# Performance work log

Hardware: AMD Instinct MI355X
Metric: run time of the kernel (lower is better)

Reference implementation:

```python
import jax, jax.numpy as jnp
import numpy as np

IN_DIM = 256
OUT_DIM = 256

def setup_inputs() -> dict:
    key = jax.random.key(0)
    k1, k2, k3, k4 = jax.random.split(key, 4)
    B, N, K, D = 4, 10000, 16, IN_DIM
    x = jax.random.normal(k1, (B, N, D), dtype=jnp.float32)
    neigh = jax.random.randint(k2, (N, K), 0, N, dtype=jnp.int64)
    # nn.Linear(2*in_dim, out_dim): W [out, 2*in], b [out]
    bound = 1.0 / np.sqrt(2 * D)
    W = jax.random.uniform(k3, (OUT_DIM, 2 * D), minval=-bound, maxval=bound, dtype=jnp.float32)
    b = jax.random.uniform(k4, (OUT_DIM,), minval=-bound, maxval=bound, dtype=jnp.float32)
    return {"x": x, "neigh": neigh, "W": W, "b": b}

def reference(x, neigh, W, b):
    # x: [B,N,D], neigh: [N,K] with -1 = padding
    mask = (neigh >= 0)                                # [N,K]
    idx = jnp.clip(neigh, 0, None)                     # [N,K]
    # batch_gather_nodes: x_nei[b,n,k,:] = x[b, idx[n,k], :]
    x_nei = x[:, idx, :]                               # [B,N,K,D]
    x_nei = x_nei * mask[None, :, :, None].astype(x.dtype)
    denom = jnp.clip(mask.sum(axis=1), 1, None).astype(x.dtype)  # [N]
    agg = x_nei.sum(axis=2) / denom[None, :, None]     # [B,N,D]
    h = jnp.concatenate([x, agg], axis=-1)             # [B,N,2D]
    return jax.nn.relu(jnp.einsum('bnd,od->bno', h, W) + b)
```

## Files before the change

kernel.cpp:

```cpp
#include <hip/hip_runtime.h>
#include <hip/hip_bf16.h>
#include <stdint.h>

#define B_   4
#define N_   10000
#define K_   16
#define D_   256
#define OUT_ 256
#define KDIM 512
#define M_   (B_ * N_)
#define CW   32
#define NCH  8

typedef __attribute__((ext_vector_type(8))) short          short8;
typedef __attribute__((ext_vector_type(8))) unsigned short ushort8;
typedef __attribute__((ext_vector_type(4))) float          f32x4;
typedef __attribute__((ext_vector_type(4))) unsigned short ushort4_t;

__device__ inline unsigned short f2bf(float f) {
    __hip_bfloat16 h = __float2bfloat16(f);
    return *reinterpret_cast<unsigned short*>(&h);
}
__device__ inline float bf2f(unsigned short u) {
    unsigned int v = ((unsigned int)u) << 16;
    return __builtin_bit_cast(float, v);
}

__global__ __launch_bounds__(256) void prep(const float* __restrict__ x,
                                            const float* __restrict__ W,
                                            unsigned short* __restrict__ h,
                                            unsigned short* __restrict__ xc,
                                            unsigned short* __restrict__ Wb) {
    const int t = threadIdx.x;
    if (blockIdx.x < 5000) {
        const int n  = blockIdx.x * 2 + (t >> 7);
        const int b  = (t >> 5) & 3;
        const int c0 = (t & 31) * 8;
        const float4* xr = (const float4*)(x + ((size_t)b * N_ + n) * D_ + c0);
        float4 v0 = xr[0];
        float4 v1 = xr[1];
        ushort8 s;
        s[0] = f2bf(v0.x); s[1] = f2bf(v0.y); s[2] = f2bf(v0.z); s[3] = f2bf(v0.w);
        s[4] = f2bf(v1.x); s[5] = f2bf(v1.y); s[6] = f2bf(v1.z); s[7] = f2bf(v1.w);
        *(ushort8*)(h + ((size_t)b * N_ + n) * KDIM + c0) = s;
        const int ch  = c0 >> 5;
        const int col = c0 & 31;
        *(ushort8*)(xc + (((size_t)ch * N_ + n) * B_ + b) * CW + col) = s;
    } else {
        int g = (blockIdx.x - 5000) * 256 + t;
        float4 v = ((const float4*)W)[g];
        ushort4_t s;
        s.x = f2bf(v.x); s.y = f2bf(v.y); s.z = f2bf(v.z); s.w = f2bf(v.w);
        ((ushort4_t*)Wb)[g] = s;
    }
}

__global__ __launch_bounds__(256) void gather_agg(const unsigned short* __restrict__ xc,
                                                  const int*            __restrict__ neigh,
                                                  unsigned short*       __restrict__ h) {
    const int c   = blockIdx.x & 7;
    const int g   = blockIdx.x >> 3;
    const int n0  = g * 8;
    const int tid = threadIdx.x;

    __shared__ int   idx_s[8 * K_];
    __shared__ float inv_s[8];

    if (tid < 8 * K_) idx_s[tid] = neigh[n0 * K_ + tid];
    __syncthreads();
    if (tid < 8) {
        int cnt = 0;
#pragma unroll
        for (int k = 0; k < K_; ++k) cnt += idx_s[tid * K_ + k] >= 0 ? 1 : 0;
        inv_s[tid] = 1.0f / (float)(cnt > 1 ? cnt : 1);
    }
    __syncthreads();

    const int q  = tid & 7;
    const int tl = tid >> 3;
    const int ns = tl >> 2;
    const int b  = tl & 3;

    const unsigned short* xcc = xc + (size_t)c * N_ * B_ * CW;

    int jj[K_];
#pragma unroll
    for (int k = 0; k < K_; ++k) jj[k] = idx_s[ns * K_ + k];

    ushort4_t vv[K_];
#pragma unroll
    for (int k = 0; k < K_; ++k) {
        const int jc = jj[k] >= 0 ? jj[k] : 0;
        vv[k] = *(const ushort4_t*)(xcc + ((size_t)jc * B_ + b) * CW + q * 4);
    }

    float a0 = 0.f, a1 = 0.f, a2 = 0.f, a3 = 0.f;
#pragma unroll
    for (int k = 0; k < K_; ++k) {
        const float m = jj[k] >= 0 ? 1.f : 0.f;
        a0 += bf2f(vv[k].x) * m;
        a1 += bf2f(vv[k].y) * m;
        a2 += bf2f(vv[k].z) * m;
        a3 += bf2f(vv[k].w) * m;
    }
    const float inv = inv_s[ns];

    ushort4_t s;
    s.x = f2bf(a0 * inv); s.y = f2bf(a1 * inv);
    s.z = f2bf(a2 * inv); s.w = f2bf(a3 * inv);
    *(ushort4_t*)(h + ((size_t)b * N_ + n0 + ns) * KDIM + D_ + c * CW + q * 4) = s;
}

__global__ __launch_bounds__(256) void gemm_bt2(const unsigned short* __restrict__ A,
                                                const unsigned short* __restrict__ Bm,
                                                const float* __restrict__ bias,
                                                float* __restrict__ out) {
    __shared__ unsigned short As[64 * 32];
    __shared__ unsigned short Bs[256 * 32];

    const int tid    = threadIdx.x;
    const int w      = tid >> 6;
    const int lane   = tid & 63;
    const int tile_m = blockIdx.x * 64;
    const int q      = lane >> 4;
    const int r16    = lane & 15;

    f32x4 acc[4][4] = {};

    const int crow = lane >> 2;
    const int kofs = (lane & 3) * 8;

    for (int kk = 0; kk < KDIM; kk += 32) {
#pragma unroll
        for (int t = 0; t < 5; ++t) {
            const int c = w * 5 + t;
            if (c < 4) {
                const int row = c * 16 + crow;
                const unsigned short* ga = A + (size_t)(tile_m + row) * KDIM + kk + kofs;
                __builtin_amdgcn_global_load_lds(
                    (const __attribute__((address_space(1))) void*)ga,
                    (__attribute__((address_space(3))) void*)(As + c * 512),
                    16, 0, 0);
            } else {
                const int row = (c - 4) * 16 + crow;
                const unsigned short* gb = Bm + (size_t)row * KDIM + kk + kofs;
                __builtin_amdgcn_global_load_lds(
                    (const __attribute__((address_space(1))) void*)gb,
                    (__attribute__((address_space(3))) void*)(Bs + (c - 4) * 512),
                    16, 0, 0);
            }
        }
        __syncthreads();

        short8 a[4], bf[4];
#pragma unroll
        for (int i = 0; i < 4; ++i)
            a[i] = *(const short8*)(As + (i * 16 + r16) * 32 + q * 8);
#pragma unroll
        for (int j = 0; j < 4; ++j)
            bf[j] = *(const short8*)(Bs + (w * 64 + j * 16 + r16) * 32 + q * 8);

#pragma unroll
        for (int i = 0; i < 4; ++i)
#pragma unroll
            for (int j = 0; j < 4; ++j)
                acc[i][j] = __builtin_amdgcn_mfma_f32_16x16x32_bf16(a[i], bf[j], acc[i][j], 0, 0, 0);

        __syncthreads();
    }

    float bj[4];
#pragma unroll
    for (int j = 0; j < 4; ++j)
        bj[j] = bias[w * 64 + j * 16 + r16];

#pragma unroll
    for (int i = 0; i < 4; ++i) {
#pragma unroll
        for (int reg = 0; reg < 4; ++reg) {
            const int m = tile_m + i * 16 + q * 4 + reg;
            float* orow = out + (size_t)m * OUT_ + w * 64;
#pragma unroll
            for (int j = 0; j < 4; ++j) {
                float v = acc[i][j][reg] + bj[j];
                orow[j * 16 + r16] = v > 0.f ? v : 0.f;
            }
        }
    }
}

extern "C" void kernel_launch(void* const* d_in, const int* in_sizes, int n_in,
                              void* d_out, int out_size, void* d_ws, size_t ws_size,
                              hipStream_t stream) {
    const float* x     = (const float*)d_in[0];
    const int*   neigh = (const int*)d_in[1];
    const float* W     = (const float*)d_in[2];
    const float* bias  = (const float*)d_in[3];
    float*       out   = (float*)d_out;

    unsigned short* Wb = (unsigned short*)d_ws;
    unsigned short* h  = Wb + OUT_ * KDIM;
    unsigned short* xc = h + (size_t)M_ * KDIM;

    prep<<<5000 + 128, 256, 0, stream>>>(x, W, h, xc, Wb);
    gather_agg<<<(N_ / 8) * NCH, 256, 0, stream>>>(xc, neigh, h);
    gemm_bt2<<<M_ / 64, 256, 0, stream>>>(h, Wb, bias, out);
}
```

Before: 140.6 us.

## Drop concatenated h buffer; GEMM reads self features and aggregate directly from global

The prep kernel no longer writes the bf16 self half of a concatenated h matrix. The GEMM now reads self features from the chunked xc layout and aggregated features from a separate hagg buffer, which removes one 20 MB bf16 write and the separate staging copy. The GEMM also drops LDS staging and __syncthreads, loading MFMA fragments straight from global memory into registers. This trades the coalesced LDS-staged loads for scattered 16-byte per-lane global loads, and W fragments are re-fetched by every block without LDS sharing.

```diff
diff --git a/kernel.cpp b/kernel.cpp
--- a/kernel.cpp
+++ b/kernel.cpp
@@ -11,6 +11,7 @@
 #define M_   (B_ * N_)
 #define CW   32
 #define NCH  8
+#define CHUNK_ELEMS ((size_t)N_ * B_ * CW)
 
 typedef __attribute__((ext_vector_type(8))) short          short8;
 typedef __attribute__((ext_vector_type(8))) unsigned short ushort8;
@@ -28,7 +29,6 @@
 
 __global__ __launch_bounds__(256) void prep(const float* __restrict__ x,
                                             const float* __restrict__ W,
-                                            unsigned short* __restrict__ h,
                                             unsigned short* __restrict__ xc,
                                             unsigned short* __restrict__ Wb) {
     const int t = threadIdx.x;
@@ -42,10 +42,9 @@
         ushort8 s;
         s[0] = f2bf(v0.x); s[1] = f2bf(v0.y); s[2] = f2bf(v0.z); s[3] = f2bf(v0.w);
         s[4] = f2bf(v1.x); s[5] = f2bf(v1.y); s[6] = f2bf(v1.z); s[7] = f2bf(v1.w);
-        *(ushort8*)(h + ((size_t)b * N_ + n) * KDIM + c0) = s;
         const int ch  = c0 >> 5;
         const int col = c0 & 31;
-        *(ushort8*)(xc + (((size_t)ch * N_ + n) * B_ + b) * CW + col) = s;
+        *(ushort8*)(xc + (size_t)ch * CHUNK_ELEMS + ((size_t)n * B_ + b) * CW + col) = s;
     } else {
         int g = (blockIdx.x - 5000) * 256 + t;
         float4 v = ((const float4*)W)[g];
@@ -57,7 +56,7 @@
 
 __global__ __launch_bounds__(256) void gather_agg(const unsigned short* __restrict__ xc,
                                                   const int*            __restrict__ neigh,
-                                                  unsigned short*       __restrict__ h) {
+                                                  unsigned short*       __restrict__ hagg) {
     const int c   = blockIdx.x & 7;
     const int g   = blockIdx.x >> 3;
     const int n0  = g * 8;
@@ -81,7 +80,7 @@
     const int ns = tl >> 2;
     const int b  = tl & 3;
 
-    const unsigned short* xcc = xc + (size_t)c * N_ * B_ * CW;
+    const unsigned short* xcc = xc + (size_t)c * CHUNK_ELEMS;
 
     int jj[K_];
 #pragma unroll
@@ -108,65 +107,68 @@
     ushort4_t s;
     s.x = f2bf(a0 * inv); s.y = f2bf(a1 * inv);
     s.z = f2bf(a2 * inv); s.w = f2bf(a3 * inv);
-    *(ushort4_t*)(h + ((size_t)b * N_ + n0 + ns) * KDIM + D_ + c * CW + q * 4) = s;
-}
-
-__global__ __launch_bounds__(256) void gemm_bt2(const unsigned short* __restrict__ A,
-                                                const unsigned short* __restrict__ Bm,
-                                                const float* __restrict__ bias,
-                                                float* __restrict__ out) {
-    __shared__ unsigned short As[64 * 32];
-    __shared__ unsigned short Bs[256 * 32];
-
+    *(ushort4_t*)(hagg + ((size_t)b * N_ + n0 + ns) * D_ + c * CW + q * 4) = s;
+}
+
+__global__ __launch_bounds__(256) void gemm_direct(const unsigned short* __restrict__ xc,
+                                                   const unsigned short* __restrict__ hagg,
+                                                   const unsigned short* __restrict__ Wb,
+                                                   const float* __restrict__ bias,
+                                                   float* __restrict__ out) {
     const int tid    = threadIdx.x;
     const int w      = tid >> 6;
     const int lane   = tid & 63;
-    const int tile_m = blockIdx.x * 64;
     const int q      = lane >> 4;
     const int r16    = lane & 15;
+    const int tile_m = blockIdx.x * 64;
+
+    const unsigned short* aself[4];
+    const unsigned short* aagg[4];
+#pragma unroll
+    for (int i = 0; i < 4; ++i) {
+        const int mi = tile_m + i * 16 + r16;
+        const int bi = (mi >= N_) + (mi >= 2 * N_) + (mi >= 3 * N_);
+        const int ni = mi - bi * N_;
+        aself[i] = xc + ((size_t)ni * B_ + bi) * CW + q * 8;
+        aagg[i]  = hagg + (size_t)mi * D_ + q * 8;
+    }
+    const unsigned short* bbase[4];
+#pragma unroll
+    for (int j = 0; j < 4; ++j)
+        bbase[j] = Wb + (size_t)(w * 64 + j * 16 + r16) * KDIM + q * 8;
 
     f32x4 acc[4][4] = {};
 
-    const int crow = lane >> 2;
-    const int kofs = (lane & 3) * 8;
-
-    for (int kk = 0; kk < KDIM; kk += 32) {
-#pragma unroll
-        for (int t = 0; t < 5; ++t) {
-            const int c = w * 5 + t;
-            if (c < 4) {
-                const int row = c * 16 + crow;
-                const unsigned short* ga = A + (size_t)(tile_m + row) * KDIM + kk + kofs;
-                __builtin_amdgcn_global_load_lds(
-                    (const __attribute__((address_space(1))) void*)ga,
-                    (__attribute__((address_space(3))) void*)(As + c * 512),
-                    16, 0, 0);
-            } else {
-                const int row = (c - 4) * 16 + crow;
-                const unsigned short* gb = Bm + (size_t)row * KDIM + kk + kofs;
-                __builtin_amdgcn_global_load_lds(
-                    (const __attribute__((address_space(1))) void*)gb,
-                    (__attribute__((address_space(3))) void*)(Bs + (c - 4) * 512),
-                    16, 0, 0);
-            }
-        }
-        __syncthreads();
-
+#pragma unroll
+    for (int c = 0; c < 8; ++c) {
         short8 a[4], bf[4];
 #pragma unroll
         for (int i = 0; i < 4; ++i)
-            a[i] = *(const short8*)(As + (i * 16 + r16) * 32 + q * 8);
+            a[i] = *(const short8*)(aself[i] + (size_t)c * CHUNK_ELEMS);
 #pragma unroll
         for (int j = 0; j < 4; ++j)
-            bf[j] = *(const short8*)(Bs + (w * 64 + j * 16 + r16) * 32 + q * 8);
-
+            bf[j] = *(const short8*)(bbase[j] + c * 32);
 #pragma unroll
         for (int i = 0; i < 4; ++i)
 #pragma unroll
             for (int j = 0; j < 4; ++j)
                 acc[i][j] = __builtin_amdgcn_mfma_f32_16x16x32_bf16(a[i], bf[j], acc[i][j], 0, 0, 0);
-
-        __syncthreads();
+    }
+
+#pragma unroll
+    for (int c = 0; c < 8; ++c) {
+        short8 a[4], bf[4];
+#pragma unroll
+        for (int i = 0; i < 4; ++i)
+            a[i] = *(const short8*)(aagg[i] + c * 32);
+#pragma unroll
+        for (int j = 0; j < 4; ++j)
+            bf[j] = *(const short8*)(bbase[j] + D_ + c * 32);
+#pragma unroll
+        for (int i = 0; i < 4; ++i)
+#pragma unroll
+            for (int j = 0; j < 4; ++j)
+                acc[i][j] = __builtin_amdgcn_mfma_f32_16x16x32_bf16(a[i], bf[j], acc[i][j], 0, 0, 0);
     }
 
     float bj[4];
@@ -198,11 +200,11 @@
     const float* bias  = (const float*)d_in[3];
     float*       out   = (float*)d_out;
 
-    unsigned short* Wb = (unsigned short*)d_ws;
-    unsigned short* h  = Wb + OUT_ * KDIM;
-    unsigned short* xc = h + (size_t)M_ * KDIM;
-
-    prep<<<5000 + 128, 256, 0, stream>>>(x, W, h, xc, Wb);
-    gather_agg<<<(N_ / 8) * NCH, 256, 0, stream>>>(xc, neigh, h);
-    gemm_bt2<<<M_ / 64, 256, 0, stream>>>(h, Wb, bias, out);
-}
+    unsigned short* Wb   = (unsigned short*)d_ws;
+    unsigned short* xc   = Wb + OUT_ * KDIM;
+    unsigned short* hagg = xc + NCH * CHUNK_ELEMS;
+
+    prep<<<5000 + 128, 256, 0, stream>>>(x, W, xc, Wb);
+    gather_agg<<<(N_ / 8) * NCH, 256, 0, stream>>>(xc, neigh, hagg);
+    gemm_direct<<<M_ / 64, 256, 0, stream>>>(xc, hagg, Wb, bias, out);
+}
```

Measured after the change: 162.5 us. 1.16x slower.

## Drop duplicate bf16 copy of x; GEMM reads self half from chunked buffer

Applied to the files above, without the earlier changes.

The prep kernel no longer writes the bf16 x into a concatenated h matrix. The GEMM now reads its first 256 K-columns straight from the chunked xc layout used by the gather, and the aggregated half from a separate hagg buffer. This removes one 20MB-class write and keeps the GEMM input split across two sources. The price is per-row address computation and A-tile loads that are less contiguous in the first half of K.

```diff
diff --git a/kernel.cpp b/kernel.cpp
--- a/kernel.cpp
+++ b/kernel.cpp
@@ -11,6 +11,7 @@
 #define M_   (B_ * N_)
 #define CW   32
 #define NCH  8
+#define CHUNK_ELEMS ((size_t)N_ * B_ * CW)
 
 typedef __attribute__((ext_vector_type(8))) short          short8;
 typedef __attribute__((ext_vector_type(8))) unsigned short ushort8;
@@ -28,7 +29,6 @@
 
 __global__ __launch_bounds__(256) void prep(const float* __restrict__ x,
                                             const float* __restrict__ W,
-                                            unsigned short* __restrict__ h,
                                             unsigned short* __restrict__ xc,
                                             unsigned short* __restrict__ Wb) {
     const int t = threadIdx.x;
@@ -42,10 +42,9 @@
         ushort8 s;
         s[0] = f2bf(v0.x); s[1] = f2bf(v0.y); s[2] = f2bf(v0.z); s[3] = f2bf(v0.w);
         s[4] = f2bf(v1.x); s[5] = f2bf(v1.y); s[6] = f2bf(v1.z); s[7] = f2bf(v1.w);
-        *(ushort8*)(h + ((size_t)b * N_ + n) * KDIM + c0) = s;
         const int ch  = c0 >> 5;
         const int col = c0 & 31;
-        *(ushort8*)(xc + (((size_t)ch * N_ + n) * B_ + b) * CW + col) = s;
+        *(ushort8*)(xc + (size_t)ch * CHUNK_ELEMS + ((size_t)n * B_ + b) * CW + col) = s;
     } else {
         int g = (blockIdx.x - 5000) * 256 + t;
         float4 v = ((const float4*)W)[g];
@@ -57,7 +56,7 @@
 
 __global__ __launch_bounds__(256) void gather_agg(const unsigned short* __restrict__ xc,
                                                   const int*            __restrict__ neigh,
-                                                  unsigned short*       __restrict__ h) {
+                                                  unsigned short*       __restrict__ hagg) {
     const int c   = blockIdx.x & 7;
     const int g   = blockIdx.x >> 3;
     const int n0  = g * 8;
@@ -81,7 +80,7 @@
     const int ns = tl >> 2;
     const int b  = tl & 3;
 
-    const unsigned short* xcc = xc + (size_t)c * N_ * B_ * CW;
+    const unsigned short* xcc = xc + (size_t)c * CHUNK_ELEMS;
 
     int jj[K_];
 #pragma unroll
@@ -108,10 +107,11 @@
     ushort4_t s;
     s.x = f2bf(a0 * inv); s.y = f2bf(a1 * inv);
     s.z = f2bf(a2 * inv); s.w = f2bf(a3 * inv);
-    *(ushort4_t*)(h + ((size_t)b * N_ + n0 + ns) * KDIM + D_ + c * CW + q * 4) = s;
-}
-
-__global__ __launch_bounds__(256) void gemm_bt2(const unsigned short* __restrict__ A,
+    *(ushort4_t*)(hagg + ((size_t)b * N_ + n0 + ns) * D_ + c * CW + q * 4) = s;
+}
+
+__global__ __launch_bounds__(256) void gemm_bt3(const unsigned short* __restrict__ xc,
+                                                const unsigned short* __restrict__ hagg,
                                                 const unsigned short* __restrict__ Bm,
                                                 const float* __restrict__ bias,
                                                 float* __restrict__ out) {
@@ -125,18 +125,31 @@
     const int q      = lane >> 4;
     const int r16    = lane & 15;
 
-    f32x4 acc[4][4] = {};
-
     const int crow = lane >> 2;
     const int kofs = (lane & 3) * 8;
 
+    const unsigned short* ps[4];
+    const unsigned short* pa[4];
+#pragma unroll
+    for (int c = 0; c < 4; ++c) {
+        const int m  = tile_m + c * 16 + crow;
+        const int b  = (m >= N_) + (m >= 2 * N_) + (m >= 3 * N_);
+        const int n  = m - b * N_;
+        ps[c] = xc + ((size_t)n * B_ + b) * CW + kofs;
+        pa[c] = hagg + (size_t)m * D_ + kofs;
+    }
+
+    f32x4 acc[4][4] = {};
+
     for (int kk = 0; kk < KDIM; kk += 32) {
+        const int kidx = kk >> 5;
 #pragma unroll
         for (int t = 0; t < 5; ++t) {
             const int c = w * 5 + t;
             if (c < 4) {
-                const int row = c * 16 + crow;
-                const unsigned short* ga = A + (size_t)(tile_m + row) * KDIM + kk + kofs;
+                const unsigned short* ga = (kk < D_)
+                    ? ps[c] + (size_t)kidx * CHUNK_ELEMS
+                    : pa[c] + (kk - D_);
                 __builtin_amdgcn_global_load_lds(
                     (const __attribute__((address_space(1))) void*)ga,
                     (__attribute__((address_space(3))) void*)(As + c * 512),
@@ -198,11 +211,11 @@
     const float* bias  = (const float*)d_in[3];
     float*       out   = (float*)d_out;
 
-    unsigned short* Wb = (unsigned short*)d_ws;
-    unsigned short* h  = Wb + OUT_ * KDIM;
-    unsigned short* xc = h + (size_t)M_ * KDIM;
-
-    prep<<<5000 + 128, 256, 0, stream>>>(x, W, h, xc, Wb);
-    gather_agg<<<(N_ / 8) * NCH, 256, 0, stream>>>(xc, neigh, h);
-    gemm_bt2<<<M_ / 64, 256, 0, stream>>>(h, Wb, bias, out);
-}
+    unsigned short* Wb   = (unsigned short*)d_ws;
+    unsigned short* xc   = Wb + OUT_ * KDIM;
+    unsigned short* hagg = xc + NCH * CHUNK_ELEMS;
+
+    prep<<<5000 + 128, 256, 0, stream>>>(x, W, xc, Wb);
+    gather_agg<<<(N_ / 8) * NCH, 256, 0, stream>>>(xc, neigh, hagg);
+    gemm_bt3<<<M_ / 64, 256, 0, stream>>>(xc, hagg, Wb, bias, out);
+}
```

After: 138.6 us. No clear change (-1.4%).
